# Kernel optimization log

Hardware: AMD Instinct MI355X
Metric: run time of the kernel (lower is better)

## Reference

```python
import jax, jax.numpy as jnp
import numpy as np

I, H, C = 128, 64, 10  # input_size, hidden_size, num_classes
B, T = 256, 1024       # batch, seq_len


def setup_inputs() -> dict:
    key = jax.random.key(0)
    ks = jax.random.split(key, 7)
    s_ih = 1.0 / np.sqrt(H)
    inp = {
        "x": jax.random.normal(ks[0], (B, T, I), dtype=jnp.float32),
        # PyTorch nn.LSTM params: gate order [i, f, g, o], each block H rows
        "W_ih": jax.random.uniform(ks[1], (4 * H, I), minval=-s_ih, maxval=s_ih, dtype=jnp.float32),
        "W_hh": jax.random.uniform(ks[2], (4 * H, H), minval=-s_ih, maxval=s_ih, dtype=jnp.float32),
        "b_ih": jax.random.uniform(ks[3], (4 * H,), minval=-s_ih, maxval=s_ih, dtype=jnp.float32),
        "b_hh": jax.random.uniform(ks[4], (4 * H,), minval=-s_ih, maxval=s_ih, dtype=jnp.float32),
        "W_cls": jax.random.uniform(ks[5], (C, H), minval=-s_ih, maxval=s_ih, dtype=jnp.float32),
        "b_cls": jax.random.uniform(ks[6], (C,), minval=-s_ih, maxval=s_ih, dtype=jnp.float32),
    }
    return inp


def _lstm_last_hidden(x, W_ih, W_hh, b_ih, b_hh):
    # Precompute input projections for all steps: (B, T, 4H)
    x_proj = jnp.einsum('bti,gi->btg', x, W_ih) + (b_ih + b_hh)
    x_proj_t = jnp.swapaxes(x_proj, 0, 1)  # (T, B, 4H) for scan over time

    def step(carry, xp_t):
        h, c = carry
        gates = xp_t + h @ W_hh.T  # (B, 4H)
        i_g, f_g, g_g, o_g = jnp.split(gates, 4, axis=-1)
        i_t = jax.nn.sigmoid(i_g)
        f_t = jax.nn.sigmoid(f_g)
        g_t = jnp.tanh(g_g)
        o_t = jax.nn.sigmoid(o_g)
        c_new = f_t * c + i_t * g_t
        h_new = o_t * jnp.tanh(c_new)
        return (h_new, c_new), None

    h0 = jnp.zeros((x.shape[0], W_hh.shape[1]), dtype=x.dtype)
    c0 = jnp.zeros_like(h0)
    (h_T, _), _ = jax.lax.scan(step, (h0, c0), x_proj_t)
    return h_T  # (B, H)


def reference(x, W_ih, W_hh, b_ih, b_hh, W_cls, b_cls):
    h_T = _lstm_last_hidden(x, W_ih, W_hh, b_ih, b_hh)
    logits = h_T @ W_cls.T + b_cls  # (B, C)
    return logits
```

## Files before the change

kernel.cpp:

```cpp
#include <hip/hip_runtime.h>


#define NI 128
#define NH 64
#define NB 256
#define NT 1024
#define NC 10

#define TT 4
#define NTILE (NT / TT)

#define LOG2E    1.44269504f
#define TWOLOG2E 2.88539008f

typedef __fp16 half2v __attribute__((ext_vector_type(2)));
typedef __fp16 f16x8  __attribute__((ext_vector_type(8)));
typedef float  f32x4  __attribute__((ext_vector_type(4)));

#define HP  80
#define XPB 268
#define XPT (4 * XPB)

#define MF(acc, a, b) \
    acc = __builtin_amdgcn_mfma_f32_16x16x32_f16(a, b, acc, 0, 0, 0)

__device__ __forceinline__ void block_sync_lds() {
    asm volatile("s_waitcnt lgkmcnt(0)\n\ts_barrier" ::: "memory");
}
__device__ __forceinline__ void wave_drain_vm() {
    asm volatile("s_waitcnt vmcnt(0)" ::: "memory");
}
__device__ __forceinline__ float fast_exp2(float x) {
#if __has_builtin(__builtin_amdgcn_exp2f)
    return __builtin_amdgcn_exp2f(x);
#else
    return __exp2f(x);
#endif
}
__device__ __forceinline__ float fast_rcp(float x) {
    return __builtin_amdgcn_rcpf(x);
}
__device__ __forceinline__ f16x8 pack8(float4 a, float4 b, float s) {
    half2v p0 = __builtin_amdgcn_cvt_pkrtz(a.x * s, a.y * s);
    half2v p1 = __builtin_amdgcn_cvt_pkrtz(a.z * s, a.w * s);
    half2v p2 = __builtin_amdgcn_cvt_pkrtz(b.x * s, b.y * s);
    half2v p3 = __builtin_amdgcn_cvt_pkrtz(b.z * s, b.w * s);
    f16x8 r;
    r[0]=p0[0]; r[1]=p0[1]; r[2]=p1[0]; r[3]=p1[1];
    r[4]=p2[0]; r[5]=p2[1]; r[6]=p3[0]; r[7]=p3[1];
    return r;
}
__device__ __forceinline__ f16x8 pack8n(float4 a, float4 b) {
    half2v p0 = __builtin_amdgcn_cvt_pkrtz(a.x, a.y);
    half2v p1 = __builtin_amdgcn_cvt_pkrtz(a.z, a.w);
    half2v p2 = __builtin_amdgcn_cvt_pkrtz(b.x, b.y);
    half2v p3 = __builtin_amdgcn_cvt_pkrtz(b.z, b.w);
    f16x8 r;
    r[0]=p0[0]; r[1]=p0[1]; r[2]=p1[0]; r[3]=p1[1];
    r[4]=p2[0]; r[5]=p2[1]; r[6]=p3[0]; r[7]=p3[1];
    return r;
}
__device__ __forceinline__ void gload_lds16(const void* g, void* l) {
    __builtin_amdgcn_global_load_lds(
        (const __attribute__((address_space(1))) unsigned int*)g,
        (__attribute__((address_space(3))) unsigned int*)l, 16, 0, 0);
}

__global__ __launch_bounds__(512, 2)
void lstm_one(const float* __restrict__ x,
              const float* __restrict__ W_ih,
              const float* __restrict__ W_hh,
              const float* __restrict__ b_ih,
              const float* __restrict__ b_hh,
              const float* __restrict__ W_cls,
              const float* __restrict__ b_cls,
              float* __restrict__ out) {
    const int tid  = threadIdx.x;
    const int w4   = tid >> 6;
    const bool cons = (w4 < 4);
    const int w    = w4 & 3;
    const int lane = tid & 63;
    const int col  = lane & 15;
    const int quad = lane >> 4;
    const int bb   = blockIdx.x;
    const int bcol = col & 3;
    const int cr   = col >> 2;

    __shared__ __align__(16) float  XS[2][4][TT * NI];
    __shared__ __align__(16) float  P[2][TT * XPT];
    __shared__ __align__(16) __fp16 H2[2][4][HP];

    if (!cons) {
        auto stage_x = [&](int tile) {
            const char* xsrc = (const char*)(x + ((size_t)(4 * bb + w) * NT
                                                  + (size_t)tile * TT) * NI);
            #pragma unroll
            for (int j = 0; j < 2; ++j) {
                const unsigned lin = j * 1024u + (unsigned)lane * 16u;
                const unsigned row = ((unsigned)w * 2048u + lin) >> 9;
                const unsigned xo  = ((row ^ (row >> 1)) & 7u) << 4;
                gload_lds16(xsrc + (lin ^ xo),
                            (char*)&XS[tile & 1][w][0] + j * 1024);
            }
        };
        stage_x(0);
        stage_x(1);

        f16x8 afrX[4][4];
        f32x4 biasf[4];
        #pragma unroll
        for (int i = 0; i < 4; ++i) {
            const int grow = 64 * i + 16 * w + col;
            const float s = (i == 2) ? TWOLOG2E : LOG2E;
            const float* Wx = W_ih + (size_t)grow * NI;
            #pragma unroll
            for (int ks = 0; ks < 4; ++ks) {
                float4 a4 = *(const float4*)(Wx + ks * 32 + quad * 8);
                float4 b4 = *(const float4*)(Wx + ks * 32 + quad * 8 + 4);
                afrX[i][ks] = pack8(a4, b4, s);
            }
            #pragma unroll
            for (int r = 0; r < 4; ++r) {
                const int u = 64 * i + 16 * w + 4 * quad + r;
                biasf[i][r] = (b_ih[u] + b_hh[u]) * s;
            }
        }

        auto produce = [&](int tp) {
            const char* XSb = (const char*)&XS[tp & 1][0][0];
            const int tl = cr;
            const unsigned row = (unsigned)(bcol * 4 + tl);
            const unsigned xo  = ((row ^ (row >> 1)) & 7u) << 4;
            const unsigned rb  = row * 512u + (unsigned)quad * 32u;
            f16x8 xb[4];
            #pragma unroll
            for (int ks = 0; ks < 4; ++ks) {
                const unsigned l0 = rb + ks * 128u;
                float4 p0 = *(const float4*)(XSb + (l0 ^ xo));
                float4 p1 = *(const float4*)(XSb + ((l0 + 16u) ^ xo));
                xb[ks] = pack8n(p0, p1);
            }
            f32x4 c0 = biasf[0], c1 = biasf[1], c2 = biasf[2], c3 = biasf[3];
            #pragma unroll
            for (int ks = 0; ks < 4; ++ks) {
                MF(c0, afrX[0][ks], xb[ks]);
                MF(c1, afrX[1][ks], xb[ks]);
                MF(c2, afrX[2][ks], xb[ks]);
                MF(c3, afrX[3][ks], xb[ks]);
            }
            float* wp = &P[tp & 1][0] + tl * XPT + bcol * XPB
                        + 16 * w + 4 * quad;
            *(f32x4*)(wp)       = c0;
            *(f32x4*)(wp + 64)  = c1;
            *(f32x4*)(wp + 128) = c2;
            *(f32x4*)(wp + 192) = c3;
        };

        wave_drain_vm();
        block_sync_lds();
        produce(0);
        block_sync_lds();

        for (int k = 0; k < NTILE; ++k) {
            if (k + 1 < NTILE) produce(k + 1);
            block_sync_lds();
            if (k + 2 < NTILE) stage_x(k + 2);
            block_sync_lds();
            block_sync_lds();
            wave_drain_vm();
            block_sync_lds();
        }
        return;
    }

    __builtin_amdgcn_s_setprio(1);

    f16x8 afrH[4][2];
    #pragma unroll
    for (int i = 0; i < 4; ++i) {
        const int grow = 64 * i + 16 * w + col;
        const float s = (i == 2) ? TWOLOG2E : LOG2E;
        const float* Wh = W_hh + (size_t)grow * NH;
        #pragma unroll
        for (int ks = 0; ks < 2; ++ks) {
            float4 a4 = *(const float4*)(Wh + ks * 32 + quad * 8);
            float4 b4 = *(const float4*)(Wh + ks * 32 + quad * 8 + 4);
            afrH[i][ks] = pack8(a4, b4, s);
        }
    }
    for (int z = tid; z < 2 * 4 * HP / 2; z += 256)
        ((unsigned*)H2)[z] = 0u;

    block_sync_lds();
    block_sync_lds();

    float c = 0.f;
    f32x4 xa0, xa1, xa2, xa3;
    auto load_xa = [&](const float* Pb, int tt) {
        const float* rp = Pb + tt * XPT + bcol * XPB + 16 * w + 4 * quad;
        xa0 = *(const f32x4*)(rp);
        xa1 = *(const f32x4*)(rp + 64);
        xa2 = *(const f32x4*)(rp + 128);
        xa3 = *(const f32x4*)(rp + 192);
    };
    load_xa(&P[0][0], 0);

    for (int k = 0; k < NTILE; ++k) {
        #pragma unroll
        for (int tt = 0; tt < TT; ++tt) {
            const int cur = tt & 1;
            const __fp16* Hc = &H2[cur][bcol][quad * 8];
            f16x8 hb0 = *(const f16x8*)(Hc);
            f16x8 hb1 = *(const f16x8*)(Hc + 32);
            f32x4 a0 = xa0, a1 = xa1, a2 = xa2, a3 = xa3;
            MF(a0, afrH[0][0], hb0);
            MF(a1, afrH[1][0], hb0);
            MF(a2, afrH[2][0], hb0);
            MF(a0, afrH[0][1], hb1);
            MF(a3, afrH[3][0], hb0);
            MF(a1, afrH[1][1], hb1);
            MF(a2, afrH[2][1], hb1);
            MF(a3, afrH[3][1], hb1);
            if (tt < TT - 1)           load_xa(&P[k & 1][0], tt + 1);
            else if (k + 1 < NTILE)    load_xa(&P[(k + 1) & 1][0], 0);
            float Ei = fast_exp2(-a0[cr]);
            float Ef = fast_exp2(-a1[cr]);
            float Eg = fast_exp2(fminf(a2[cr], 60.f));
            float Eo = fast_exp2(-a3[cr]);
            float ig = (Eg - 1.f) * fast_rcp((1.f + Ei) * (1.f + Eg));
            float fv = fast_rcp(1.f + Ef);
            c = fmaf(fv, c, ig);
            float Ec = fast_exp2(fminf(TWOLOG2E * c, 60.f));
            float h  = (Ec - 1.f) * fast_rcp((1.f + Eo) * (1.f + Ec));
            H2[cur ^ 1][bcol][16 * w + 4 * quad + cr] = (__fp16)h;
            block_sync_lds();
        }
    }

    if (tid < 4 * NC) {
        const int bl = tid / NC, cl = tid % NC;
        float acc = b_cls[cl];
        const float* wc = W_cls + cl * NH;
        #pragma unroll 8
        for (int k = 0; k < NH; ++k)
            acc = fmaf(wc[k], (float)H2[0][bl][k], acc);
        out[(4 * bb + bl) * NC + cl] = acc;
    }
}

extern "C" void kernel_launch(void* const* d_in, const int* in_sizes, int n_in,
                              void* d_out, int out_size, void* d_ws, size_t ws_size,
                              hipStream_t stream) {
    const float* x     = (const float*)d_in[0];
    const float* W_ih  = (const float*)d_in[1];
    const float* W_hh  = (const float*)d_in[2];
    const float* b_ih  = (const float*)d_in[3];
    const float* b_hh  = (const float*)d_in[4];
    const float* W_cls = (const float*)d_in[5];
    const float* b_cls = (const float*)d_in[6];
    float* out = (float*)d_out;

    lstm_one<<<NB / 4, 512, 0, stream>>>(x, W_ih, W_hh, b_ih, b_hh,
                                         W_cls, b_cls, out);
}
```

Baseline: 447.2 us.

## Merge producer waves into consumer waves, interleaving input projection with recurrence

```diff
diff --git a/kernel.cpp b/kernel.cpp
--- a/kernel.cpp
+++ b/kernel.cpp
@@ -66,7 +66,7 @@
         (__attribute__((address_space(3))) unsigned int*)l, 16, 0, 0);
 }
 
-__global__ __launch_bounds__(512, 2)
+__global__ __launch_bounds__(256, 1)
 void lstm_one(const float* __restrict__ x,
               const float* __restrict__ W_ih,
               const float* __restrict__ W_hh,
@@ -76,9 +76,7 @@
               const float* __restrict__ b_cls,
               float* __restrict__ out) {
     const int tid  = threadIdx.x;
-    const int w4   = tid >> 6;
-    const bool cons = (w4 < 4);
-    const int w    = w4 & 3;
+    const int w    = tid >> 6;
     const int lane = tid & 63;
     const int col  = lane & 15;
     const int quad = lane >> 4;
@@ -90,96 +88,35 @@
     __shared__ __align__(16) float  P[2][TT * XPT];
     __shared__ __align__(16) __fp16 H2[2][4][HP];
 
-    if (!cons) {
-        auto stage_x = [&](int tile) {
-            const char* xsrc = (const char*)(x + ((size_t)(4 * bb + w) * NT
-                                                  + (size_t)tile * TT) * NI);
-            #pragma unroll
-            for (int j = 0; j < 2; ++j) {
-                const unsigned lin = j * 1024u + (unsigned)lane * 16u;
-                const unsigned row = ((unsigned)w * 2048u + lin) >> 9;
-                const unsigned xo  = ((row ^ (row >> 1)) & 7u) << 4;
-                gload_lds16(xsrc + (lin ^ xo),
-                            (char*)&XS[tile & 1][w][0] + j * 1024);
-            }
-        };
-        stage_x(0);
-        stage_x(1);
-
-        f16x8 afrX[4][4];
-        f32x4 biasf[4];
-        #pragma unroll
-        for (int i = 0; i < 4; ++i) {
-            const int grow = 64 * i + 16 * w + col;
-            const float s = (i == 2) ? TWOLOG2E : LOG2E;
-            const float* Wx = W_ih + (size_t)grow * NI;
-            #pragma unroll
-            for (int ks = 0; ks < 4; ++ks) {
-                float4 a4 = *(const float4*)(Wx + ks * 32 + quad * 8);
-                float4 b4 = *(const float4*)(Wx + ks * 32 + quad * 8 + 4);
-                afrX[i][ks] = pack8(a4, b4, s);
-            }
-            #pragma unroll
-            for (int r = 0; r < 4; ++r) {
-                const int u = 64 * i + 16 * w + 4 * quad + r;
-                biasf[i][r] = (b_ih[u] + b_hh[u]) * s;
-            }
-        }
-
-        auto produce = [&](int tp) {
-            const char* XSb = (const char*)&XS[tp & 1][0][0];
-            const int tl = cr;
-            const unsigned row = (unsigned)(bcol * 4 + tl);
+    auto stage_x = [&](int tile) {
+        const char* xsrc = (const char*)(x + ((size_t)(4 * bb + w) * NT
+                                              + (size_t)tile * TT) * NI);
+        #pragma unroll
+        for (int j = 0; j < 2; ++j) {
+            const unsigned lin = j * 1024u + (unsigned)lane * 16u;
+            const unsigned row = ((unsigned)w * 2048u + lin) >> 9;
             const unsigned xo  = ((row ^ (row >> 1)) & 7u) << 4;
-            const unsigned rb  = row * 512u + (unsigned)quad * 32u;
-            f16x8 xb[4];
-            #pragma unroll
-            for (int ks = 0; ks < 4; ++ks) {
-                const unsigned l0 = rb + ks * 128u;
-                float4 p0 = *(const float4*)(XSb + (l0 ^ xo));
-                float4 p1 = *(const float4*)(XSb + ((l0 + 16u) ^ xo));
-                xb[ks] = pack8n(p0, p1);
-            }
-            f32x4 c0 = biasf[0], c1 = biasf[1], c2 = biasf[2], c3 = biasf[3];
-            #pragma unroll
-            for (int ks = 0; ks < 4; ++ks) {
-                MF(c0, afrX[0][ks], xb[ks]);
-                MF(c1, afrX[1][ks], xb[ks]);
-                MF(c2, afrX[2][ks], xb[ks]);
-                MF(c3, afrX[3][ks], xb[ks]);
-            }
-            float* wp = &P[tp & 1][0] + tl * XPT + bcol * XPB
-                        + 16 * w + 4 * quad;
-            *(f32x4*)(wp)       = c0;
-            *(f32x4*)(wp + 64)  = c1;
-            *(f32x4*)(wp + 128) = c2;
-            *(f32x4*)(wp + 192) = c3;
-        };
-
-        wave_drain_vm();
-        block_sync_lds();
-        produce(0);
-        block_sync_lds();
-
-        for (int k = 0; k < NTILE; ++k) {
-            if (k + 1 < NTILE) produce(k + 1);
-            block_sync_lds();
-            if (k + 2 < NTILE) stage_x(k + 2);
-            block_sync_lds();
-            block_sync_lds();
-            wave_drain_vm();
-            block_sync_lds();
-        }
-        return;
-    }
-
-    __builtin_amdgcn_s_setprio(1);
-
+            gload_lds16(xsrc + (lin ^ xo),
+                        (char*)&XS[tile & 1][w][0] + j * 1024);
+        }
+    };
+    stage_x(0);
+    stage_x(1);
+
+    f16x8 afrX[4][4];
     f16x8 afrH[4][2];
+    f32x4 biasf[4];
     #pragma unroll
     for (int i = 0; i < 4; ++i) {
         const int grow = 64 * i + 16 * w + col;
         const float s = (i == 2) ? TWOLOG2E : LOG2E;
+        const float* Wx = W_ih + (size_t)grow * NI;
+        #pragma unroll
+        for (int ks = 0; ks < 4; ++ks) {
+            float4 a4 = *(const float4*)(Wx + ks * 32 + quad * 8);
+            float4 b4 = *(const float4*)(Wx + ks * 32 + quad * 8 + 4);
+            afrX[i][ks] = pack8(a4, b4, s);
+        }
         const float* Wh = W_hh + (size_t)grow * NH;
         #pragma unroll
         for (int ks = 0; ks < 2; ++ks) {
@@ -187,11 +124,46 @@
             float4 b4 = *(const float4*)(Wh + ks * 32 + quad * 8 + 4);
             afrH[i][ks] = pack8(a4, b4, s);
         }
+        #pragma unroll
+        for (int r = 0; r < 4; ++r) {
+            const int u = 64 * i + 16 * w + 4 * quad + r;
+            biasf[i][r] = (b_ih[u] + b_hh[u]) * s;
+        }
     }
     for (int z = tid; z < 2 * 4 * HP / 2; z += 256)
         ((unsigned*)H2)[z] = 0u;
 
+    const unsigned rowP = (unsigned)(bcol * 4 + cr);
+    const unsigned xoP  = ((rowP ^ (rowP >> 1)) & 7u) << 4;
+    const unsigned rbP  = rowP * 512u + (unsigned)quad * 32u;
+
+    wave_drain_vm();
     block_sync_lds();
+
+    {
+        const char* XSb = (const char*)&XS[0][0][0];
+        f16x8 xb[4];
+        #pragma unroll
+        for (int ks = 0; ks < 4; ++ks) {
+            const unsigned l0 = rbP + ks * 128u;
+            float4 p0 = *(const float4*)(XSb + (l0 ^ xoP));
+            float4 p1 = *(const float4*)(XSb + ((l0 + 16u) ^ xoP));
+            xb[ks] = pack8n(p0, p1);
+        }
+        f32x4 c0 = biasf[0], c1 = biasf[1], c2 = biasf[2], c3 = biasf[3];
+        #pragma unroll
+        for (int ks = 0; ks < 4; ++ks) {
+            MF(c0, afrX[0][ks], xb[ks]);
+            MF(c1, afrX[1][ks], xb[ks]);
+            MF(c2, afrX[2][ks], xb[ks]);
+            MF(c3, afrX[3][ks], xb[ks]);
+        }
+        float* wp = &P[0][0] + cr * XPT + bcol * XPB + 16 * w + 4 * quad;
+        *(f32x4*)(wp)       = c0;
+        *(f32x4*)(wp + 64)  = c1;
+        *(f32x4*)(wp + 128) = c2;
+        *(f32x4*)(wp + 192) = c3;
+    }
     block_sync_lds();
 
     float c = 0.f;
@@ -206,26 +178,55 @@
     load_xa(&P[0][0], 0);
 
     for (int k = 0; k < NTILE; ++k) {
+        const int doP = (k + 1 < NTILE);
+        const char* XSn = (const char*)&XS[(k + 1) & 1][0][0];
+        f32x4 pc0, pc1, pc2, pc3;
         #pragma unroll
         for (int tt = 0; tt < TT; ++tt) {
             const int cur = tt & 1;
             const __fp16* Hc = &H2[cur][bcol][quad * 8];
             f16x8 hb0 = *(const f16x8*)(Hc);
             f16x8 hb1 = *(const f16x8*)(Hc + 32);
+            float4 q0, q1;
+            if (doP) {
+                const unsigned l0 = rbP + (unsigned)tt * 128u;
+                q0 = *(const float4*)(XSn + (l0 ^ xoP));
+                q1 = *(const float4*)(XSn + ((l0 + 16u) ^ xoP));
+            }
+            if (tt == 0 && k + 2 < NTILE) stage_x(k + 2);
             f32x4 a0 = xa0, a1 = xa1, a2 = xa2, a3 = xa3;
+            MF(a2, afrH[2][0], hb0);
             MF(a0, afrH[0][0], hb0);
             MF(a1, afrH[1][0], hb0);
-            MF(a2, afrH[2][0], hb0);
+            MF(a3, afrH[3][0], hb0);
+            MF(a2, afrH[2][1], hb1);
             MF(a0, afrH[0][1], hb1);
-            MF(a3, afrH[3][0], hb0);
             MF(a1, afrH[1][1], hb1);
-            MF(a2, afrH[2][1], hb1);
             MF(a3, afrH[3][1], hb1);
-            if (tt < TT - 1)           load_xa(&P[k & 1][0], tt + 1);
-            else if (k + 1 < NTILE)    load_xa(&P[(k + 1) & 1][0], 0);
+            if (doP) {
+                if (tt == 0) {
+                    pc0 = biasf[0]; pc1 = biasf[1];
+                    pc2 = biasf[2]; pc3 = biasf[3];
+                }
+                f16x8 xbv = pack8n(q0, q1);
+                MF(pc0, afrX[0][tt], xbv);
+                MF(pc1, afrX[1][tt], xbv);
+                MF(pc2, afrX[2][tt], xbv);
+                MF(pc3, afrX[3][tt], xbv);
+                if (tt == TT - 1) {
+                    float* wp = &P[(k + 1) & 1][0] + cr * XPT + bcol * XPB
+                                + 16 * w + 4 * quad;
+                    *(f32x4*)(wp)       = pc0;
+                    *(f32x4*)(wp + 64)  = pc1;
+                    *(f32x4*)(wp + 128) = pc2;
+                    *(f32x4*)(wp + 192) = pc3;
+                }
+            }
+            if (tt < TT - 1)  load_xa(&P[k & 1][0], tt + 1);
+            else if (doP)     load_xa(&P[(k + 1) & 1][0], 0);
+            float Eg = fast_exp2(fminf(a2[cr], 60.f));
             float Ei = fast_exp2(-a0[cr]);
             float Ef = fast_exp2(-a1[cr]);
-            float Eg = fast_exp2(fminf(a2[cr], 60.f));
             float Eo = fast_exp2(-a3[cr]);
             float ig = (Eg - 1.f) * fast_rcp((1.f + Ei) * (1.f + Eg));
             float fv = fast_rcp(1.f + Ef);
@@ -233,6 +234,7 @@
             float Ec = fast_exp2(fminf(TWOLOG2E * c, 60.f));
             float h  = (Ec - 1.f) * fast_rcp((1.f + Eo) * (1.f + Ec));
             H2[cur ^ 1][bcol][16 * w + 4 * quad + cr] = (__fp16)h;
+            if (tt == TT - 1) wave_drain_vm();
             block_sync_lds();
         }
     }
@@ -260,6 +262,6 @@
     const float* b_cls = (const float*)d_in[6];
     float* out = (float*)d_out;
 
-    lstm_one<<<NB / 4, 512, 0, stream>>>(x, W_ih, W_hh, b_ih, b_hh,
+    lstm_one<<<NB / 4, 256, 0, stream>>>(x, W_ih, W_hh, b_ih, b_hh,
                                          W_cls, b_cls, out);
 }
```

Measured after the change: 620.5 us. 38.8% more time.
